# Optimization experiments

Measured on AMD Instinct MI355X. Metric: run time of the kernel, lower is better.

Reference implementation:

```python
import jax, jax.numpy as jnp
import numpy as np

N = 20000      # nodes
G = 400        # distinct TCR group ids
D_IN, H1, H2, D_OUT = 128, 256, 256, 128
LN_EPS = 1e-5


def _init_linear(key, fan_in, fan_out):
    s = 1.0 / np.sqrt(fan_in)
    return jax.random.uniform(key, (fan_in, fan_out), jnp.float32, -s, s)


def setup_inputs() -> dict:
    key = jax.random.key(0)
    ks = jax.random.split(key, 6)
    x = jax.random.normal(ks[0], (N, D_IN), jnp.float32)
    idx_TCR = jax.random.randint(ks[1], (N,), 0, G, dtype=jnp.int64)
    W1 = _init_linear(ks[2], D_IN, H1)
    W2 = _init_linear(ks[3], H1, H2)
    W3 = _init_linear(ks[4], H2, D_OUT)
    b1 = jnp.zeros((H1,), jnp.float32)
    b2 = jnp.zeros((H2,), jnp.float32)
    b3 = jnp.zeros((D_OUT,), jnp.float32)
    gamma = jnp.ones((D_OUT,), jnp.float32)
    beta = jnp.zeros((D_OUT,), jnp.float32)
    return {"x": x, "idx_TCR": idx_TCR, "W1": W1, "b1": b1,
            "W2": W2, "b2": b2, "W3": W3, "b3": b3,
            "gamma": gamma, "beta": beta}


def _build_edges(idx_TCR):
    # construct_graph: connect node pairs with equal idx, upper triangle only
    # (directed src<tgt edges, as in the torch code), then append self-loops
    # as PyG GCNConv.gcn_norm does.
    idx = np.asarray(idx_TCR).reshape(-1)
    n = idx.shape[0]
    eq = idx[:, None] == idx[None, :]
    src, tgt = np.nonzero(np.triu(eq, k=1))
    loop = np.arange(n)
    row = jnp.asarray(np.concatenate([src, loop]))  # message source
    col = jnp.asarray(np.concatenate([tgt, loop]))  # message target
    return row, col, n


def _gcn_norm(row, col, n, dtype):
    # degree from incoming edges (incl. self-loops), symmetric normalization
    deg = jax.ops.segment_sum(jnp.ones(row.shape[0], dtype), col, num_segments=n)
    dis = jnp.where(deg > 0, jax.lax.rsqrt(deg), jnp.zeros_like(deg))
    return dis[row] * dis[col]  # [E]


def _gcn_conv(x, W, b, row, col, norm, n):
    h = x @ W                                   # [N, out]
    msg = h[row] * norm[:, None]                # gather + scale, [E, out]
    out = jax.ops.segment_sum(msg, col, num_segments=n)  # scatter-add
    return out + b


def reference(x, idx_TCR, W1, b1, W2, b2, W3, b3, gamma, beta):
    row, col, n = _build_edges(idx_TCR)
    norm = _gcn_norm(row, col, n, x.dtype)
    h = jax.nn.relu(_gcn_conv(x, W1, b1, row, col, norm, n))
    h = jax.nn.relu(_gcn_conv(h, W2, b2, row, col, norm, n))
    h = jax.nn.relu(_gcn_conv(h, W3, b3, row, col, norm, n))
    # LayerNorm over last dim
    mu = h.mean(axis=-1, keepdims=True)
    var = ((h - mu) ** 2).mean(axis=-1, keepdims=True)
    return (h - mu) * jax.lax.rsqrt(var + LN_EPS) * gamma + beta
```

## Files before the change

### kernel.cpp

```cpp
#include <hip/hip_runtime.h>
#include <hip/hip_bf16.h>

#define NN 20000
#define NG 400
#define D_IN 128
#define H1 256
#define H2 256
#define D_OUT 128
#define MCAP 1024
#define WSLOT 256

#define STY 72
#define ST1 136
#define ST2 264
#define ST3 264
#define SF  132
#define REGB 36864

typedef __attribute__((ext_vector_type(8))) short short8;
typedef __attribute__((ext_vector_type(4))) short short4v;
typedef __attribute__((ext_vector_type(4))) float floatx4;

__device__ __forceinline__ short f2b(float f) {
    __hip_bfloat16 h = __float2bfloat16(f);
    return *(short*)&h;
}


__global__ __launch_bounds__(256) void wt_all_t(
    const float* __restrict__ W1, const float* __restrict__ W2,
    const float* __restrict__ W3, __hip_bfloat16* __restrict__ Wt1,
    __hip_bfloat16* __restrict__ Wt2, __hip_bfloat16* __restrict__ Wt3)
{
    __shared__ float tile[64][65];

    int bid = blockIdx.x;
    const float* W; __hip_bfloat16* Wt; int K, N, tk, tn;
    if (bid < 8)       { W = W1; Wt = Wt1; K = D_IN; N = H1;
                         tk = bid >> 2;        tn = bid & 3; }
    else if (bid < 24) { W = W2; Wt = Wt2; K = H1;   N = H2;
                         int b = bid - 8;  tk = b >> 2; tn = b & 3; }
    else               { W = W3; Wt = Wt3; K = H2;   N = D_OUT;
                         int b = bid - 24; tk = b >> 1; tn = b & 1; }

    int t = threadIdx.x;
    int c = t & 63;
    int r0 = t >> 6;
    int k0 = tk * 64, n0 = tn * 64;

#pragma unroll
    for (int it = 0; it < 16; ++it) {
        int r = r0 + it * 4;
        tile[r][c] = W[(size_t)(k0 + r) * N + n0 + c];
    }
    __syncthreads();

#pragma unroll
    for (int it = 0; it < 16; ++it) {
        int rn = r0 + it * 4;
        Wt[(size_t)(n0 + rn) * K + k0 + c] = __float2bfloat16(tile[c][rn]);
    }
}


__global__ __launch_bounds__(512) void fused_gcn(
    const float* __restrict__ x, const int* __restrict__ idx,
    const __hip_bfloat16* __restrict__ Wt1_,
    const __hip_bfloat16* __restrict__ Wt2_,
    const __hip_bfloat16* __restrict__ Wt3_,
    const float* __restrict__ b1, const float* __restrict__ b2,
    const float* __restrict__ b3,
    const float* __restrict__ gamma, const float* __restrict__ beta,
    float* __restrict__ out)
{
    __shared__ __align__(16) char RA[REGB];
    __shared__ __align__(16) char RB[REGB];
    __shared__ int mlist[MCAP];
    __shared__ int wcnt[8];

    int tid = threadIdx.x;
    int w = tid >> 6;
    int lane = tid & 63;
    int quad = lane >> 4;
    int l15 = lane & 15;
    int g = blockIdx.x;

    int* WS = (int*)RA;
    {
        int slice = w * 625;
        int wcount = 0;
        unsigned long long lowm = (1ull << lane) - 1ull;
#pragma unroll
        for (int b2i = 0; b2i < 2; ++b2i) {
            int4 v[5];
#pragma unroll
            for (int r = 0; r < 5; ++r) {
                int q = (b2i * 5 + r) * 64 + lane;
                v[r] = (q < 625) ? *(const int4*)&idx[(slice + q) * 4]
                                 : make_int4(-1, -1, -1, -1);
            }
#pragma unroll
            for (int r = 0; r < 5; ++r) {
                bool f0 = (v[r].x == g), f1 = (v[r].y == g);
                bool f2 = (v[r].z == g), f3 = (v[r].w == g);
                unsigned long long m0 = __ballot(f0), m1 = __ballot(f1);
                unsigned long long m2 = __ballot(f2), m3 = __ballot(f3);
                int p = wcount + __popcll(m0 & lowm) + __popcll(m1 & lowm)
                               + __popcll(m2 & lowm) + __popcll(m3 & lowm);
                int j0 = (slice + (b2i * 5 + r) * 64 + lane) * 4;
                int e0 = (int)f0, e1 = (int)f1, e2 = (int)f2;
                if (f0 && p < WSLOT)                WS[w * WSLOT + p] = j0;
                if (f1 && p + e0 < WSLOT)           WS[w * WSLOT + p + e0] = j0 + 1;
                if (f2 && p + e0 + e1 < WSLOT)      WS[w * WSLOT + p + e0 + e1] = j0 + 2;
                if (f3 && p + e0 + e1 + e2 < WSLOT) WS[w * WSLOT + p + e0 + e1 + e2] = j0 + 3;
                wcount += __popcll(m0) + __popcll(m1) + __popcll(m2) + __popcll(m3);
            }
        }
        if (lane == 0) wcnt[w] = min(wcount, WSLOT);
    }
    __syncthreads();
    int cnt = 0;
    {
        int myprefix = 0;
#pragma unroll
        for (int ww = 0; ww < 8; ++ww) {
            int c = wcnt[ww];
            if (ww < w) myprefix += c;
            cnt += c;
        }
        cnt = min(cnt, MCAP);
        int myc = wcnt[w];
        for (int k = lane; k < myc; k += 64) {
            int dstp = myprefix + k;
            if (dstp < MCAP) mlist[dstp] = WS[w * WSLOT + k];
        }
    }
    if (cnt <= 0) return;

    float2 gmv = *(const float2*)&gamma[lane * 2];
    float2 btv = *(const float2*)&beta[lane * 2];
    float4 bb1[2], bb2[2], bb3;
#pragma unroll
    for (int i = 0; i < 2; ++i) {
        bb1[i] = *(const float4*)&b1[(2 * w + i) * 16 + quad * 4];
        bb2[i] = *(const float4*)&b2[(2 * w + i) * 16 + quad * 4];
    }
    bb3 = *(const float4*)&b3[w * 16 + quad * 4];

    __syncthreads();

    auto ltfrag = [&](int nt, int k2) -> short8 {
        int thr = nt * 16 + l15 - k2 * 32 - quad * 8;
        short8 f;
#pragma unroll
        for (int e = 0; e < 8; ++e)
            f[e] = (e <= thr) ? (short)0x3F80 : (short)0;
        return f;
    };

    float c1[2][4], c2[2][4], c3[4];
#pragma unroll
    for (int r = 0; r < 4; ++r) {
        c1[0][r] = 0.f; c1[1][r] = 0.f;
        c2[0][r] = 0.f; c2[1][r] = 0.f;
        c3[r] = 0.f;
    }

    const short* wt1p = (const short*)Wt1_;
    const short* wt2p = (const short*)Wt2_;
    const short* wt3p = (const short*)Wt3_;

    for (int base = 0; base < cnt; base += 64) {
        asm("" : "+s"(wt1p), "+s"(wt2p), "+s"(wt3p));
        int mt = min(64, cnt - base);
        int par = (base >> 6) & 1;
        char* Rc = par ? RB : RA;
        char* Rd = par ? RA : RB;
        short* T1 = (short*)Rc;
        short* T2 = (short*)Rc;
        short* T3 = (short*)Rc;
        float* F  = (float*)Rc;
        short* Yt = (short*)Rd;

        float djn[4];
#pragma unroll
        for (int nt = 0; nt < 4; ++nt)
            djn[nt] = rsqrtf((float)(base + nt * 16 + l15 + 1));

        {
            int row = (lane >> 3) + 8 * w;
            int mr = base + row;
            int nid = mlist[mr < cnt ? mr : cnt - 1];
            float sdr = rsqrtf((float)(mr + 1));
            const float* xp = x + (size_t)nid * D_IN + (lane & 7) * 4;
#pragma unroll
            for (int t = 0; t < 4; ++t) {
                float4 v = *(const float4*)(xp + t * 32);
                short4v o;
                o[0] = f2b(v.x * sdr); o[1] = f2b(v.y * sdr);
                o[2] = f2b(v.z * sdr); o[3] = f2b(v.w * sdr);
                *(short4v*)&T1[row * ST1 + (lane & 7) * 4 + t * 32] = o;
            }
        }
        __syncthreads();

        {
            floatx4 acc[4][2];
#pragma unroll
            for (int i = 0; i < 4; ++i) { acc[i][0] = (floatx4)0.0f; acc[i][1] = (floatx4)0.0f; }
#pragma unroll
            for (int kk = 0; kk < 4; ++kk) {
                short8 a4[4], bw[2];
#pragma unroll
                for (int i = 0; i < 4; ++i)
                    a4[i] = *(const short8*)&T1[(i * 16 + l15) * ST1 + kk * 32 + quad * 8];
#pragma unroll
                for (int nt = 0; nt < 2; ++nt)
                    bw[nt] = *(const short8*)&wt1p[((size_t)((w * 2 + nt) * 16 + l15)) * D_IN + kk * 32 + quad * 8];
#pragma unroll
                for (int i = 0; i < 4; ++i)
#pragma unroll
                    for (int nt = 0; nt < 2; ++nt)
                        acc[i][nt] = __builtin_amdgcn_mfma_f32_16x16x32_bf16(
                            a4[i], bw[nt], acc[i][nt], 0, 0, 0);
            }
#pragma unroll
            for (int i = 0; i < 4; ++i)
#pragma unroll
                for (int nt = 0; nt < 2; ++nt) {
                    short4v o4;
#pragma unroll
                    for (int r = 0; r < 4; ++r) o4[r] = f2b(acc[i][nt][r]);
                    *(short4v*)&Yt[((w * 2 + nt) * 16 + l15) * STY + i * 16 + quad * 4] = o4;
                }
        }
        __syncthreads();

        {
            floatx4 acc[2][4];
#pragma unroll
            for (int i = 0; i < 2; ++i)
#pragma unroll
                for (int nt = 0; nt < 4; ++nt) acc[i][nt] = (floatx4)0.0f;
#pragma unroll
            for (int k2 = 0; k2 < 2; ++k2) {
                short8 af[2];
#pragma unroll
                for (int i = 0; i < 2; ++i)
                    af[i] = *(const short8*)&Yt[((2 * w + i) * 16 + l15) * STY + k2 * 32 + quad * 8];
#pragma unroll
                for (int nt = 0; nt < 4; ++nt) {
                    short8 lt = ltfrag(nt, k2);
#pragma unroll
                    for (int i = 0; i < 2; ++i)
                        acc[i][nt] = __builtin_amdgcn_mfma_f32_16x16x32_bf16(
                            af[i], lt, acc[i][nt], 0, 0, 0);
                }
            }
#pragma unroll
            for (int i = 0; i < 2; ++i) {
                float nc[4] = {0.f, 0.f, 0.f, 0.f};
#pragma unroll
                for (int nt = 0; nt < 4; ++nt) {
                    float tmp[4];
#pragma unroll
                    for (int r = 0; r < 4; ++r) tmp[r] = acc[i][nt][r] + c1[i][r];
                    if (nt == 3) {
#pragma unroll
                        for (int r = 0; r < 4; ++r) nc[r] = tmp[r];
                    }
                    short4v o4;
                    o4[0] = f2b(fmaxf(tmp[0] * djn[nt] + bb1[i].x, 0.0f) * djn[nt]);
                    o4[1] = f2b(fmaxf(tmp[1] * djn[nt] + bb1[i].y, 0.0f) * djn[nt]);
                    o4[2] = f2b(fmaxf(tmp[2] * djn[nt] + bb1[i].z, 0.0f) * djn[nt]);
                    o4[3] = f2b(fmaxf(tmp[3] * djn[nt] + bb1[i].w, 0.0f) * djn[nt]);
                    *(short4v*)&T2[(nt * 16 + l15) * ST2 + (2 * w + i) * 16 + quad * 4] = o4;
                }
#pragma unroll
                for (int r = 0; r < 4; ++r)
                    c1[i][r] = __shfl(nc[r], (lane & 48) + 15);
            }
        }
        __syncthreads();

        {
            floatx4 acc[4][2];
#pragma unroll
            for (int i = 0; i < 4; ++i) { acc[i][0] = (floatx4)0.0f; acc[i][1] = (floatx4)0.0f; }
#pragma unroll
            for (int kk = 0; kk < 8; ++kk) {
                short8 a4[4], bw[2];
#pragma unroll
                for (int i = 0; i < 4; ++i)
                    a4[i] = *(const short8*)&T2[(i * 16 + l15) * ST2 + kk * 32 + quad * 8];
#pragma unroll
                for (int nt = 0; nt < 2; ++nt)
                    bw[nt] = *(const short8*)&wt2p[((size_t)((w * 2 + nt) * 16 + l15)) * H1 + kk * 32 + quad * 8];
#pragma unroll
                for (int i = 0; i < 4; ++i)
#pragma unroll
                    for (int nt = 0; nt < 2; ++nt)
                        acc[i][nt] = __builtin_amdgcn_mfma_f32_16x16x32_bf16(
                            a4[i], bw[nt], acc[i][nt], 0, 0, 0);
            }
#pragma unroll
            for (int i = 0; i < 4; ++i)
#pragma unroll
                for (int nt = 0; nt < 2; ++nt) {
                    short4v o4;
#pragma unroll
                    for (int r = 0; r < 4; ++r) o4[r] = f2b(acc[i][nt][r]);
                    *(short4v*)&Yt[((w * 2 + nt) * 16 + l15) * STY + i * 16 + quad * 4] = o4;
                }
        }
        __syncthreads();

        {
            floatx4 acc[2][4];
#pragma unroll
            for (int i = 0; i < 2; ++i)
#pragma unroll
                for (int nt = 0; nt < 4; ++nt) acc[i][nt] = (floatx4)0.0f;
#pragma unroll
            for (int k2 = 0; k2 < 2; ++k2) {
                short8 af[2];
#pragma unroll
                for (int i = 0; i < 2; ++i)
                    af[i] = *(const short8*)&Yt[((2 * w + i) * 16 + l15) * STY + k2 * 32 + quad * 8];
#pragma unroll
                for (int nt = 0; nt < 4; ++nt) {
                    short8 lt = ltfrag(nt, k2);
#pragma unroll
                    for (int i = 0; i < 2; ++i)
                        acc[i][nt] = __builtin_amdgcn_mfma_f32_16x16x32_bf16(
                            af[i], lt, acc[i][nt], 0, 0, 0);
                }
            }
#pragma unroll
            for (int i = 0; i < 2; ++i) {
                float nc[4] = {0.f, 0.f, 0.f, 0.f};
#pragma unroll
                for (int nt = 0; nt < 4; ++nt) {
                    float tmp[4];
#pragma unroll
                    for (int r = 0; r < 4; ++r) tmp[r] = acc[i][nt][r] + c2[i][r];
                    if (nt == 3) {
#pragma unroll
                        for (int r = 0; r < 4; ++r) nc[r] = tmp[r];
                    }
                    short4v o4;
                    o4[0] = f2b(fmaxf(tmp[0] * djn[nt] + bb2[i].x, 0.0f) * djn[nt]);
                    o4[1] = f2b(fmaxf(tmp[1] * djn[nt] + bb2[i].y, 0.0f) * djn[nt]);
                    o4[2] = f2b(fmaxf(tmp[2] * djn[nt] + bb2[i].z, 0.0f) * djn[nt]);
                    o4[3] = f2b(fmaxf(tmp[3] * djn[nt] + bb2[i].w, 0.0f) * djn[nt]);
                    *(short4v*)&T3[(nt * 16 + l15) * ST3 + (2 * w + i) * 16 + quad * 4] = o4;
                }
#pragma unroll
                for (int r = 0; r < 4; ++r)
                    c2[i][r] = __shfl(nc[r], (lane & 48) + 15);
            }
        }
        __syncthreads();

        {
            floatx4 acc[4];
#pragma unroll
            for (int i = 0; i < 4; ++i) acc[i] = (floatx4)0.0f;
#pragma unroll
            for (int kk = 0; kk < 8; ++kk) {
                short8 bw = *(const short8*)&wt3p[((size_t)(w * 16 + l15)) * H2 + kk * 32 + quad * 8];
#pragma unroll
                for (int i = 0; i < 4; ++i) {
                    short8 a4 = *(const short8*)&T3[(i * 16 + l15) * ST3 + kk * 32 + quad * 8];
                    acc[i] = __builtin_amdgcn_mfma_f32_16x16x32_bf16(a4, bw, acc[i], 0, 0, 0);
                }
            }
#pragma unroll
            for (int i = 0; i < 4; ++i) {
                short4v o4;
#pragma unroll
                for (int r = 0; r < 4; ++r) o4[r] = f2b(acc[i][r]);
                *(short4v*)&Yt[(w * 16 + l15) * STY + i * 16 + quad * 4] = o4;
            }
        }
        __syncthreads();

        {
            floatx4 acc[4];
#pragma unroll
            for (int nt = 0; nt < 4; ++nt) acc[nt] = (floatx4)0.0f;
#pragma unroll
            for (int k2 = 0; k2 < 2; ++k2) {
                short8 af = *(const short8*)&Yt[(w * 16 + l15) * STY + k2 * 32 + quad * 8];
#pragma unroll
                for (int nt = 0; nt < 4; ++nt)
                    acc[nt] = __builtin_amdgcn_mfma_f32_16x16x32_bf16(
                        af, ltfrag(nt, k2), acc[nt], 0, 0, 0);
            }
            float nc[4] = {0.f, 0.f, 0.f, 0.f};
#pragma unroll
            for (int nt = 0; nt < 4; ++nt) {
                float tmp[4];
#pragma unroll
                for (int r = 0; r < 4; ++r) tmp[r] = acc[nt][r] + c3[r];
                if (nt == 3) {
#pragma unroll
                    for (int r = 0; r < 4; ++r) nc[r] = tmp[r];
                }
                float4 o;
                o.x = fmaxf(tmp[0] * djn[nt] + bb3.x, 0.0f);
                o.y = fmaxf(tmp[1] * djn[nt] + bb3.y, 0.0f);
                o.z = fmaxf(tmp[2] * djn[nt] + bb3.z, 0.0f);
                o.w = fmaxf(tmp[3] * djn[nt] + bb3.w, 0.0f);
                *(float4*)&F[(nt * 16 + l15) * SF + w * 16 + quad * 4] = o;
            }
#pragma unroll
            for (int r = 0; r < 4; ++r)
                c3[r] = __shfl(nc[r], (lane & 48) + 15);
        }
        __syncthreads();

        for (int r = w; r < mt; r += 8) {
            float2 v = *(const float2*)&F[r * SF + lane * 2];
            float s1 = v.x + v.y;
            float s2v = v.x * v.x + v.y * v.y;
#pragma unroll
            for (int off = 32; off > 0; off >>= 1) {
                s1 += __shfl_down(s1, off);
                s2v += __shfl_down(s2v, off);
            }
            s1 = __shfl(s1, 0);
            s2v = __shfl(s2v, 0);
            float mu = s1 * (1.0f / D_OUT);
            float var = s2v * (1.0f / D_OUT) - mu * mu;
            float rstd = rsqrtf(var + 1e-5f);
            float2 o;
            o.x = (v.x - mu) * rstd * gmv.x + btv.x;
            o.y = (v.y - mu) * rstd * gmv.y + btv.y;
            *(float2*)&out[(size_t)mlist[base + r] * D_OUT + lane * 2] = o;
        }
    }
}


extern "C" void kernel_launch(void* const* d_in, const int* in_sizes, int n_in,
                              void* d_out, int out_size, void* d_ws, size_t ws_size,
                              hipStream_t stream) {
    const float* x     = (const float*)d_in[0];
    const int*   idx   = (const int*)d_in[1];
    const float* W1    = (const float*)d_in[2];
    const float* b1    = (const float*)d_in[3];
    const float* W2    = (const float*)d_in[4];
    const float* b2    = (const float*)d_in[5];
    const float* W3    = (const float*)d_in[6];
    const float* b3    = (const float*)d_in[7];
    const float* gamma = (const float*)d_in[8];
    const float* beta  = (const float*)d_in[9];
    float* out = (float*)d_out;

    char* ws = (char*)d_ws;
    size_t off = 0;
    auto alloc = [&](size_t bytes) -> void* {
        void* p = (void*)(ws + off);
        off += (bytes + 255) & ~(size_t)255;
        return p;
    };
    __hip_bfloat16* Wt1 = (__hip_bfloat16*)alloc((size_t)D_IN * H1 * 2);
    __hip_bfloat16* Wt2 = (__hip_bfloat16*)alloc((size_t)H1 * H2 * 2);
    __hip_bfloat16* Wt3 = (__hip_bfloat16*)alloc((size_t)H2 * D_OUT * 2);

    wt_all_t<<<32, 256, 0, stream>>>(W1, W2, W3, Wt1, Wt2, Wt3);

    fused_gcn<<<NG, 512, 0, stream>>>(
        x, idx, Wt1, Wt2, Wt3, b1, b2, b3, gamma, beta, out);
}
```

Baseline: 127.4 us.

## Switch to persistent blocks with atomic work-stealing over TCR groups

Launches 256 persistent blocks instead of one block per group. After finishing a group, each block grabs the next group index from a global atomic counter that is zeroed by a memset before launch. This is meant to cut tail effects and per-block launch and setup costs across the 400 groups of uneven size. In exchange it adds a memset, one atomic per group and extra barriers, and every group still rescans the whole index array.

After: 127.9 us. No clear change (+0.4%).

```diff
diff --git a/kernel.cpp b/kernel.cpp
--- a/kernel.cpp
+++ b/kernel.cpp
@@ -9,6 +9,7 @@
 #define D_OUT 128
 #define MCAP 1024
 #define WSLOT 256
+#define GRID0 256
 
 #define STY 72
 #define ST1 136
@@ -54,7 +55,6 @@
         tile[r][c] = W[(size_t)(k0 + r) * N + n0 + c];
     }
     __syncthreads();
-
 #pragma unroll
     for (int it = 0; it < 16; ++it) {
         int rn = r0 + it * 4;
@@ -71,83 +71,27 @@
     const float* __restrict__ b1, const float* __restrict__ b2,
     const float* __restrict__ b3,
     const float* __restrict__ gamma, const float* __restrict__ beta,
-    float* __restrict__ out)
+    float* __restrict__ out, int* __restrict__ gctr)
 {
     __shared__ __align__(16) char RA[REGB];
     __shared__ __align__(16) char RB[REGB];
     __shared__ int mlist[MCAP];
     __shared__ int wcnt[8];
+    __shared__ int gsh;
 
     int tid = threadIdx.x;
     int w = tid >> 6;
     int lane = tid & 63;
     int quad = lane >> 4;
     int l15 = lane & 15;
-    int g = blockIdx.x;
-
-    int* WS = (int*)RA;
-    {
-        int slice = w * 625;
-        int wcount = 0;
-        unsigned long long lowm = (1ull << lane) - 1ull;
-#pragma unroll
-        for (int b2i = 0; b2i < 2; ++b2i) {
-            int4 v[5];
-#pragma unroll
-            for (int r = 0; r < 5; ++r) {
-                int q = (b2i * 5 + r) * 64 + lane;
-                v[r] = (q < 625) ? *(const int4*)&idx[(slice + q) * 4]
-                                 : make_int4(-1, -1, -1, -1);
-            }
-#pragma unroll
-            for (int r = 0; r < 5; ++r) {
-                bool f0 = (v[r].x == g), f1 = (v[r].y == g);
-                bool f2 = (v[r].z == g), f3 = (v[r].w == g);
-                unsigned long long m0 = __ballot(f0), m1 = __ballot(f1);
-                unsigned long long m2 = __ballot(f2), m3 = __ballot(f3);
-                int p = wcount + __popcll(m0 & lowm) + __popcll(m1 & lowm)
-                               + __popcll(m2 & lowm) + __popcll(m3 & lowm);
-                int j0 = (slice + (b2i * 5 + r) * 64 + lane) * 4;
-                int e0 = (int)f0, e1 = (int)f1, e2 = (int)f2;
-                if (f0 && p < WSLOT)                WS[w * WSLOT + p] = j0;
-                if (f1 && p + e0 < WSLOT)           WS[w * WSLOT + p + e0] = j0 + 1;
-                if (f2 && p + e0 + e1 < WSLOT)      WS[w * WSLOT + p + e0 + e1] = j0 + 2;
-                if (f3 && p + e0 + e1 + e2 < WSLOT) WS[w * WSLOT + p + e0 + e1 + e2] = j0 + 3;
-                wcount += __popcll(m0) + __popcll(m1) + __popcll(m2) + __popcll(m3);
-            }
-        }
-        if (lane == 0) wcnt[w] = min(wcount, WSLOT);
-    }
-    __syncthreads();
-    int cnt = 0;
-    {
-        int myprefix = 0;
-#pragma unroll
-        for (int ww = 0; ww < 8; ++ww) {
-            int c = wcnt[ww];
-            if (ww < w) myprefix += c;
-            cnt += c;
-        }
-        cnt = min(cnt, MCAP);
-        int myc = wcnt[w];
-        for (int k = lane; k < myc; k += 64) {
-            int dstp = myprefix + k;
-            if (dstp < MCAP) mlist[dstp] = WS[w * WSLOT + k];
-        }
-    }
-    if (cnt <= 0) return;
 
     float2 gmv = *(const float2*)&gamma[lane * 2];
     float2 btv = *(const float2*)&beta[lane * 2];
-    float4 bb1[2], bb2[2], bb3;
-#pragma unroll
-    for (int i = 0; i < 2; ++i) {
-        bb1[i] = *(const float4*)&b1[(2 * w + i) * 16 + quad * 4];
-        bb2[i] = *(const float4*)&b2[(2 * w + i) * 16 + quad * 4];
-    }
-    bb3 = *(const float4*)&b3[w * 16 + quad * 4];
-
-    __syncthreads();
+    float4 bb1a = *(const float4*)&b1[(2 * w + 0) * 16 + quad * 4];
+    float4 bb1b = *(const float4*)&b1[(2 * w + 1) * 16 + quad * 4];
+    float4 bb2a = *(const float4*)&b2[(2 * w + 0) * 16 + quad * 4];
+    float4 bb2b = *(const float4*)&b2[(2 * w + 1) * 16 + quad * 4];
+    float4 bb3  = *(const float4*)&b3[w * 16 + quad * 4];
 
     auto ltfrag = [&](int nt, int k2) -> short8 {
         int thr = nt * 16 + l15 - k2 * 32 - quad * 8;
@@ -158,287 +102,353 @@
         return f;
     };
 
-    float c1[2][4], c2[2][4], c3[4];
-#pragma unroll
-    for (int r = 0; r < 4; ++r) {
-        c1[0][r] = 0.f; c1[1][r] = 0.f;
-        c2[0][r] = 0.f; c2[1][r] = 0.f;
-        c3[r] = 0.f;
-    }
-
     const short* wt1p = (const short*)Wt1_;
     const short* wt2p = (const short*)Wt2_;
     const short* wt3p = (const short*)Wt3_;
 
-    for (int base = 0; base < cnt; base += 64) {
-        asm("" : "+s"(wt1p), "+s"(wt2p), "+s"(wt3p));
-        int mt = min(64, cnt - base);
-        int par = (base >> 6) & 1;
-        char* Rc = par ? RB : RA;
-        char* Rd = par ? RA : RB;
-        short* T1 = (short*)Rc;
-        short* T2 = (short*)Rc;
-        short* T3 = (short*)Rc;
-        float* F  = (float*)Rc;
-        short* Yt = (short*)Rd;
-
-        float djn[4];
-#pragma unroll
-        for (int nt = 0; nt < 4; ++nt)
-            djn[nt] = rsqrtf((float)(base + nt * 16 + l15 + 1));
-
+    int g = blockIdx.x;
+    while (g < NG) {
+        __syncthreads();
+
+        int* WS = (int*)RA;
         {
-            int row = (lane >> 3) + 8 * w;
-            int mr = base + row;
-            int nid = mlist[mr < cnt ? mr : cnt - 1];
-            float sdr = rsqrtf((float)(mr + 1));
-            const float* xp = x + (size_t)nid * D_IN + (lane & 7) * 4;
-#pragma unroll
-            for (int t = 0; t < 4; ++t) {
-                float4 v = *(const float4*)(xp + t * 32);
-                short4v o;
-                o[0] = f2b(v.x * sdr); o[1] = f2b(v.y * sdr);
-                o[2] = f2b(v.z * sdr); o[3] = f2b(v.w * sdr);
-                *(short4v*)&T1[row * ST1 + (lane & 7) * 4 + t * 32] = o;
+            int slice = w * 625;
+            int wcount = 0;
+            unsigned long long lowm = (1ull << lane) - 1ull;
+#pragma unroll
+            for (int b2i = 0; b2i < 2; ++b2i) {
+                int4 v[5];
+#pragma unroll
+                for (int r = 0; r < 5; ++r) {
+                    int q = (b2i * 5 + r) * 64 + lane;
+                    v[r] = (q < 625) ? *(const int4*)&idx[(slice + q) * 4]
+                                     : make_int4(-1, -1, -1, -1);
+                }
+#pragma unroll
+                for (int r = 0; r < 5; ++r) {
+                    bool f0 = (v[r].x == g), f1 = (v[r].y == g);
+                    bool f2 = (v[r].z == g), f3 = (v[r].w == g);
+                    unsigned long long m0 = __ballot(f0), m1 = __ballot(f1);
+                    unsigned long long m2 = __ballot(f2), m3 = __ballot(f3);
+                    int p = wcount + __popcll(m0 & lowm) + __popcll(m1 & lowm)
+                                   + __popcll(m2 & lowm) + __popcll(m3 & lowm);
+                    int j0 = (slice + (b2i * 5 + r) * 64 + lane) * 4;
+                    int e0 = (int)f0, e1 = (int)f1, e2 = (int)f2;
+                    if (f0 && p < WSLOT)                WS[w * WSLOT + p] = j0;
+                    if (f1 && p + e0 < WSLOT)           WS[w * WSLOT + p + e0] = j0 + 1;
+                    if (f2 && p + e0 + e1 < WSLOT)      WS[w * WSLOT + p + e0 + e1] = j0 + 2;
+                    if (f3 && p + e0 + e1 + e2 < WSLOT) WS[w * WSLOT + p + e0 + e1 + e2] = j0 + 3;
+                    wcount += __popcll(m0) + __popcll(m1) + __popcll(m2) + __popcll(m3);
+                }
+            }
+            if (lane == 0) wcnt[w] = min(wcount, WSLOT);
+        }
+        __syncthreads();
+        int cnt = 0;
+        {
+            int myprefix = 0;
+#pragma unroll
+            for (int ww = 0; ww < 8; ++ww) {
+                int c = wcnt[ww];
+                if (ww < w) myprefix += c;
+                cnt += c;
+            }
+            cnt = min(cnt, MCAP);
+            int myc = wcnt[w];
+            for (int k = lane; k < myc; k += 64) {
+                int dstp = myprefix + k;
+                if (dstp < MCAP) mlist[dstp] = WS[w * WSLOT + k];
             }
         }
-        __syncthreads();
-
-        {
-            floatx4 acc[4][2];
-#pragma unroll
-            for (int i = 0; i < 4; ++i) { acc[i][0] = (floatx4)0.0f; acc[i][1] = (floatx4)0.0f; }
-#pragma unroll
-            for (int kk = 0; kk < 4; ++kk) {
-                short8 a4[4], bw[2];
-#pragma unroll
-                for (int i = 0; i < 4; ++i)
-                    a4[i] = *(const short8*)&T1[(i * 16 + l15) * ST1 + kk * 32 + quad * 8];
-#pragma unroll
-                for (int nt = 0; nt < 2; ++nt)
-                    bw[nt] = *(const short8*)&wt1p[((size_t)((w * 2 + nt) * 16 + l15)) * D_IN + kk * 32 + quad * 8];
-#pragma unroll
-                for (int i = 0; i < 4; ++i)
-#pragma unroll
-                    for (int nt = 0; nt < 2; ++nt)
-                        acc[i][nt] = __builtin_amdgcn_mfma_f32_16x16x32_bf16(
-                            a4[i], bw[nt], acc[i][nt], 0, 0, 0);
+
+        if (cnt > 0) {
+            __syncthreads();
+
+            float c1[2][4], c2[2][4], c3[4];
+#pragma unroll
+            for (int r = 0; r < 4; ++r) {
+                c1[0][r] = 0.f; c1[1][r] = 0.f;
+                c2[0][r] = 0.f; c2[1][r] = 0.f;
+                c3[r] = 0.f;
             }
-#pragma unroll
-            for (int i = 0; i < 4; ++i)
-#pragma unroll
-                for (int nt = 0; nt < 2; ++nt) {
-                    short4v o4;
-#pragma unroll
-                    for (int r = 0; r < 4; ++r) o4[r] = f2b(acc[i][nt][r]);
-                    *(short4v*)&Yt[((w * 2 + nt) * 16 + l15) * STY + i * 16 + quad * 4] = o4;
-                }
-        }
-        __syncthreads();
-
-        {
-            floatx4 acc[2][4];
-#pragma unroll
-            for (int i = 0; i < 2; ++i)
-#pragma unroll
-                for (int nt = 0; nt < 4; ++nt) acc[i][nt] = (floatx4)0.0f;
-#pragma unroll
-            for (int k2 = 0; k2 < 2; ++k2) {
-                short8 af[2];
-#pragma unroll
-                for (int i = 0; i < 2; ++i)
-                    af[i] = *(const short8*)&Yt[((2 * w + i) * 16 + l15) * STY + k2 * 32 + quad * 8];
-#pragma unroll
-                for (int nt = 0; nt < 4; ++nt) {
-                    short8 lt = ltfrag(nt, k2);
+            float4 bb1[2] = {bb1a, bb1b};
+            float4 bb2[2] = {bb2a, bb2b};
+
+            for (int base = 0; base < cnt; base += 64) {
+                asm("" : "+s"(wt1p), "+s"(wt2p), "+s"(wt3p));
+                int mt = min(64, cnt - base);
+                int par = (base >> 6) & 1;
+                char* Rc = par ? RB : RA;
+                char* Rd = par ? RA : RB;
+                short* T1 = (short*)Rc;
+                short* T2 = (short*)Rc;
+                short* T3 = (short*)Rc;
+                float* F  = (float*)Rc;
+                short* Yt = (short*)Rd;
+
+                float djn[4];
+#pragma unroll
+                for (int nt = 0; nt < 4; ++nt)
+                    djn[nt] = rsqrtf((float)(base + nt * 16 + l15 + 1));
+
+                {
+                    int row = (lane >> 3) + 8 * w;
+                    int mr = base + row;
+                    int nid = mlist[mr < cnt ? mr : cnt - 1];
+                    float sdr = rsqrtf((float)(mr + 1));
+                    const float* xp = x + (size_t)nid * D_IN + (lane & 7) * 4;
+#pragma unroll
+                    for (int t = 0; t < 4; ++t) {
+                        float4 v = *(const float4*)(xp + t * 32);
+                        short4v o;
+                        o[0] = f2b(v.x * sdr); o[1] = f2b(v.y * sdr);
+                        o[2] = f2b(v.z * sdr); o[3] = f2b(v.w * sdr);
+                        *(short4v*)&T1[row * ST1 + (lane & 7) * 4 + t * 32] = o;
+                    }
+                }
+                __syncthreads();
+
+                {
+                    floatx4 acc[4][2];
+#pragma unroll
+                    for (int i = 0; i < 4; ++i) { acc[i][0] = (floatx4)0.0f; acc[i][1] = (floatx4)0.0f; }
+#pragma unroll
+                    for (int kk = 0; kk < 4; ++kk) {
+                        short8 a4[4], bw[2];
+#pragma unroll
+                        for (int i = 0; i < 4; ++i)
+                            a4[i] = *(const short8*)&T1[(i * 16 + l15) * ST1 + kk * 32 + quad * 8];
+#pragma unroll
+                        for (int nt = 0; nt < 2; ++nt)
+                            bw[nt] = *(const short8*)&wt1p[((size_t)((w * 2 + nt) * 16 + l15)) * D_IN + kk * 32 + quad * 8];
+#pragma unroll
+                        for (int i = 0; i < 4; ++i)
+#pragma unroll
+                            for (int nt = 0; nt < 2; ++nt)
+                                acc[i][nt] = __builtin_amdgcn_mfma_f32_16x16x32_bf16(
+                                    a4[i], bw[nt], acc[i][nt], 0, 0, 0);
+                    }
+#pragma unroll
+                    for (int i = 0; i < 4; ++i)
+#pragma unroll
+                        for (int nt = 0; nt < 2; ++nt) {
+                            short4v o4;
+#pragma unroll
+                            for (int r = 0; r < 4; ++r) o4[r] = f2b(acc[i][nt][r]);
+                            *(short4v*)&Yt[((w * 2 + nt) * 16 + l15) * STY + i * 16 + quad * 4] = o4;
+                        }
+                }
+                __syncthreads();
+
+                {
+                    floatx4 acc[2][4];
 #pragma unroll
                     for (int i = 0; i < 2; ++i)
-                        acc[i][nt] = __builtin_amdgcn_mfma_f32_16x16x32_bf16(
-                            af[i], lt, acc[i][nt], 0, 0, 0);
-                }
-            }
-#pragma unroll
-            for (int i = 0; i < 2; ++i) {
-                float nc[4] = {0.f, 0.f, 0.f, 0.f};
-#pragma unroll
-                for (int nt = 0; nt < 4; ++nt) {
-                    float tmp[4];
-#pragma unroll
-                    for (int r = 0; r < 4; ++r) tmp[r] = acc[i][nt][r] + c1[i][r];
-                    if (nt == 3) {
-#pragma unroll
-                        for (int r = 0; r < 4; ++r) nc[r] = tmp[r];
-                    }
-                    short4v o4;
-                    o4[0] = f2b(fmaxf(tmp[0] * djn[nt] + bb1[i].x, 0.0f) * djn[nt]);
-                    o4[1] = f2b(fmaxf(tmp[1] * djn[nt] + bb1[i].y, 0.0f) * djn[nt]);
-                    o4[2] = f2b(fmaxf(tmp[2] * djn[nt] + bb1[i].z, 0.0f) * djn[nt]);
-                    o4[3] = f2b(fmaxf(tmp[3] * djn[nt] + bb1[i].w, 0.0f) * djn[nt]);
-                    *(short4v*)&T2[(nt * 16 + l15) * ST2 + (2 * w + i) * 16 + quad * 4] = o4;
-                }
-#pragma unroll
-                for (int r = 0; r < 4; ++r)
-                    c1[i][r] = __shfl(nc[r], (lane & 48) + 15);
+#pragma unroll
+                        for (int nt = 0; nt < 4; ++nt) acc[i][nt] = (floatx4)0.0f;
+#pragma unroll
+                    for (int k2 = 0; k2 < 2; ++k2) {
+                        short8 af[2];
+#pragma unroll
+                        for (int i = 0; i < 2; ++i)
+                            af[i] = *(const short8*)&Yt[((2 * w + i) * 16 + l15) * STY + k2 * 32 + quad * 8];
+#pragma unroll
+                        for (int nt = 0; nt < 4; ++nt) {
+                            short8 lt = ltfrag(nt, k2);
+#pragma unroll
+                            for (int i = 0; i < 2; ++i)
+                                acc[i][nt] = __builtin_amdgcn_mfma_f32_16x16x32_bf16(
+                                    af[i], lt, acc[i][nt], 0, 0, 0);
+                        }
+                    }
+#pragma unroll
+                    for (int i = 0; i < 2; ++i) {
+                        float nc[4] = {0.f, 0.f, 0.f, 0.f};
+#pragma unroll
+                        for (int nt = 0; nt < 4; ++nt) {
+                            float tmp[4];
+#pragma unroll
+                            for (int r = 0; r < 4; ++r) tmp[r] = acc[i][nt][r] + c1[i][r];
+                            if (nt == 3) {
+#pragma unroll
+                                for (int r = 0; r < 4; ++r) nc[r] = tmp[r];
+                            }
+                            short4v o4;
+                            o4[0] = f2b(fmaxf(tmp[0] * djn[nt] + bb1[i].x, 0.0f) * djn[nt]);
+                            o4[1] = f2b(fmaxf(tmp[1] * djn[nt] + bb1[i].y, 0.0f) * djn[nt]);
+                            o4[2] = f2b(fmaxf(tmp[2] * djn[nt] + bb1[i].z, 0.0f) * djn[nt]);
+                            o4[3] = f2b(fmaxf(tmp[3] * djn[nt] + bb1[i].w, 0.0f) * djn[nt]);
+                            *(short4v*)&T2[(nt * 16 + l15) * ST2 + (2 * w + i) * 16 + quad * 4] = o4;
+                        }
+#pragma unroll
+                        for (int r = 0; r < 4; ++r)
+                            c1[i][r] = __shfl(nc[r], (lane & 48) + 15);
+                    }
+                }
+                __syncthreads();
+
+                {
+                    floatx4 acc[4][2];
+#pragma unroll
+                    for (int i = 0; i < 4; ++i) { acc[i][0] = (floatx4)0.0f; acc[i][1] = (floatx4)0.0f; }
+#pragma unroll
+                    for (int kk = 0; kk < 8; ++kk) {
+                        short8 a4[4], bw[2];
+#pragma unroll
+                        for (int i = 0; i < 4; ++i)
+                            a4[i] = *(const short8*)&T2[(i * 16 + l15) * ST2 + kk * 32 + quad * 8];
+#pragma unroll
+                        for (int nt = 0; nt < 2; ++nt)
+                            bw[nt] = *(const short8*)&wt2p[((size_t)((w * 2 + nt) * 16 + l15)) * H1 + kk * 32 + quad * 8];
+#pragma unroll
+                        for (int i = 0; i < 4; ++i)
+#pragma unroll
+                            for (int nt = 0; nt < 2; ++nt)
+                                acc[i][nt] = __builtin_amdgcn_mfma_f32_16x16x32_bf16(
+                                    a4[i], bw[nt], acc[i][nt], 0, 0, 0);
+                    }
+#pragma unroll
+                    for (int i = 0; i < 4; ++i)
+#pragma unroll
+                        for (int nt = 0; nt < 2; ++nt) {
+                            short4v o4;
+#pragma unroll
+                            for (int r = 0; r < 4; ++r) o4[r] = f2b(acc[i][nt][r]);
+                            *(short4v*)&Yt[((w * 2 + nt) * 16 + l15) * STY + i * 16 + quad * 4] = o4;
+                        }
+                }
+                __syncthreads();
+
+                {
+                    floatx4 acc[2][4];
+#pragma unroll
+                    for (int i = 0; i < 2; ++i)
+#pragma unroll
+                        for (int nt = 0; nt < 4; ++nt) acc[i][nt] = (floatx4)0.0f;
+#pragma unroll
+                    for (int k2 = 0; k2 < 2; ++k2) {
+                        short8 af[2];
+#pragma unroll
+                        for (int i = 0; i < 2; ++i)
+                            af[i] = *(const short8*)&Yt[((2 * w + i) * 16 + l15) * STY + k2 * 32 + quad * 8];
+#pragma unroll
+                        for (int nt = 0; nt < 4; ++nt) {
+                            short8 lt = ltfrag(nt, k2);
+#pragma unroll
+                            for (int i = 0; i < 2; ++i)
+                                acc[i][nt] = __builtin_amdgcn_mfma_f32_16x16x32_bf16(
+                                    af[i], lt, acc[i][nt], 0, 0, 0);
+                        }
+                    }
+#pragma unroll
+                    for (int i = 0; i < 2; ++i) {
+                        float nc[4] = {0.f, 0.f, 0.f, 0.f};
+#pragma unroll
+                        for (int nt = 0; nt < 4; ++nt) {
+                            float tmp[4];
+#pragma unroll
+                            for (int r = 0; r < 4; ++r) tmp[r] = acc[i][nt][r] + c2[i][r];
+                            if (nt == 3) {
+#pragma unroll
+                                for (int r = 0; r < 4; ++r) nc[r] = tmp[r];
+                            }
+                            short4v o4;
+                            o4[0] = f2b(fmaxf(tmp[0] * djn[nt] + bb2[i].x, 0.0f) * djn[nt]);
+                            o4[1] = f2b(fmaxf(tmp[1] * djn[nt] + bb2[i].y, 0.0f) * djn[nt]);
+                            o4[2] = f2b(fmaxf(tmp[2] * djn[nt] + bb2[i].z, 0.0f) * djn[nt]);
+                            o4[3] = f2b(fmaxf(tmp[3] * djn[nt] + bb2[i].w, 0.0f) * djn[nt]);
+                            *(short4v*)&T3[(nt * 16 + l15) * ST3 + (2 * w + i) * 16 + quad * 4] = o4;
+                        }
+#pragma unroll
+                        for (int r = 0; r < 4; ++r)
+                            c2[i][r] = __shfl(nc[r], (lane & 48) + 15);
+                    }
+                }
+                __syncthreads();
+
+                {
+                    floatx4 acc[4];
+#pragma unroll
+                    for (int i = 0; i < 4; ++i) acc[i] = (floatx4)0.0f;
+#pragma unroll
+                    for (int kk = 0; kk < 8; ++kk) {
+                        short8 bw = *(const short8*)&wt3p[((size_t)(w * 16 + l15)) * H2 + kk * 32 + quad * 8];
+#pragma unroll
+                        for (int i = 0; i < 4; ++i) {
+                            short8 a4 = *(const short8*)&T3[(i * 16 + l15) * ST3 + kk * 32 + quad * 8];
+                            acc[i] = __builtin_amdgcn_mfma_f32_16x16x32_bf16(a4, bw, acc[i], 0, 0, 0);
+                        }
+                    }
+#pragma unroll
+                    for (int i = 0; i < 4; ++i) {
+                        short4v o4;
+#pragma unroll
+                        for (int r = 0; r < 4; ++r) o4[r] = f2b(acc[i][r]);
+                        *(short4v*)&Yt[(w * 16 + l15) * STY + i * 16 + quad * 4] = o4;
+                    }
+                }
+                __syncthreads();
+
+                {
+                    floatx4 acc[4];
+#pragma unroll
+                    for (int nt = 0; nt < 4; ++nt) acc[nt] = (floatx4)0.0f;
+#pragma unroll
+                    for (int k2 = 0; k2 < 2; ++k2) {
+                        short8 af = *(const short8*)&Yt[(w * 16 + l15) * STY + k2 * 32 + quad * 8];
+#pragma unroll
+                        for (int nt = 0; nt < 4; ++nt)
+                            acc[nt] = __builtin_amdgcn_mfma_f32_16x16x32_bf16(
+                                af, ltfrag(nt, k2), acc[nt], 0, 0, 0);
+                    }
+                    float nc[4] = {0.f, 0.f, 0.f, 0.f};
+#pragma unroll
+                    for (int nt = 0; nt < 4; ++nt) {
+                        float tmp[4];
+#pragma unroll
+                        for (int r = 0; r < 4; ++r) tmp[r] = acc[nt][r] + c3[r];
+                        if (nt == 3) {
+#pragma unroll
+                            for (int r = 0; r < 4; ++r) nc[r] = tmp[r];
+                        }
+                        float4 o;
+                        o.x = fmaxf(tmp[0] * djn[nt] + bb3.x, 0.0f);
+                        o.y = fmaxf(tmp[1] * djn[nt] + bb3.y, 0.0f);
+                        o.z = fmaxf(tmp[2] * djn[nt] + bb3.z, 0.0f);
+                        o.w = fmaxf(tmp[3] * djn[nt] + bb3.w, 0.0f);
+                        *(float4*)&F[(nt * 16 + l15) * SF + w * 16 + quad * 4] = o;
+                    }
+#pragma unroll
+                    for (int r = 0; r < 4; ++r)
+                        c3[r] = __shfl(nc[r], (lane & 48) + 15);
+                }
+                __syncthreads();
+
+                for (int r = w; r < mt; r += 8) {
+                    float2 v = *(const float2*)&F[r * SF + lane * 2];
+                    float s1 = v.x + v.y;
+                    float s2v = v.x * v.x + v.y * v.y;
+#pragma unroll
+                    for (int off = 32; off > 0; off >>= 1) {
+                        s1 += __shfl_down(s1, off);
+                        s2v += __shfl_down(s2v, off);
+                    }
+                    s1 = __shfl(s1, 0);
+                    s2v = __shfl(s2v, 0);
+                    float mu = s1 * (1.0f / D_OUT);
+                    float var = s2v * (1.0f / D_OUT) - mu * mu;
+                    float rstd = rsqrtf(var + 1e-5f);
+                    float2 o;
+                    o.x = (v.x - mu) * rstd * gmv.x + btv.x;
+                    o.y = (v.y - mu) * rstd * gmv.y + btv.y;
+                    *(float2*)&out[(size_t)mlist[base + r] * D_OUT + lane * 2] = o;
+                }
             }
         }
+
+        if (tid == 0) gsh = GRID0 + atomicAdd(gctr, 1);
         __syncthreads();
-
-        {
-            floatx4 acc[4][2];
-#pragma unroll
-            for (int i = 0; i < 4; ++i) { acc[i][0] = (floatx4)0.0f; acc[i][1] = (floatx4)0.0f; }
-#pragma unroll
-            for (int kk = 0; kk < 8; ++kk) {
-                short8 a4[4], bw[2];
-#pragma unroll
-                for (int i = 0; i < 4; ++i)
-                    a4[i] = *(const short8*)&T2[(i * 16 + l15) * ST2 + kk * 32 + quad * 8];
-#pragma unroll
-                for (int nt = 0; nt < 2; ++nt)
-                    bw[nt] = *(const short8*)&wt2p[((size_t)((w * 2 + nt) * 16 + l15)) * H1 + kk * 32 + quad * 8];
-#pragma unroll
-                for (int i = 0; i < 4; ++i)
-#pragma unroll
-                    for (int nt = 0; nt < 2; ++nt)
-                        acc[i][nt] = __builtin_amdgcn_mfma_f32_16x16x32_bf16(
-                            a4[i], bw[nt], acc[i][nt], 0, 0, 0);
-            }
-#pragma unroll
-            for (int i = 0; i < 4; ++i)
-#pragma unroll
-                for (int nt = 0; nt < 2; ++nt) {
-                    short4v o4;
-#pragma unroll
-                    for (int r = 0; r < 4; ++r) o4[r] = f2b(acc[i][nt][r]);
-                    *(short4v*)&Yt[((w * 2 + nt) * 16 + l15) * STY + i * 16 + quad * 4] = o4;
-                }
-        }
-        __syncthreads();
-
-        {
-            floatx4 acc[2][4];
-#pragma unroll
-            for (int i = 0; i < 2; ++i)
-#pragma unroll
-                for (int nt = 0; nt < 4; ++nt) acc[i][nt] = (floatx4)0.0f;
-#pragma unroll
-            for (int k2 = 0; k2 < 2; ++k2) {
-                short8 af[2];
-#pragma unroll
-                for (int i = 0; i < 2; ++i)
-                    af[i] = *(const short8*)&Yt[((2 * w + i) * 16 + l15) * STY + k2 * 32 + quad * 8];
-#pragma unroll
-                for (int nt = 0; nt < 4; ++nt) {
-                    short8 lt = ltfrag(nt, k2);
-#pragma unroll
-                    for (int i = 0; i < 2; ++i)
-                        acc[i][nt] = __builtin_amdgcn_mfma_f32_16x16x32_bf16(
-                            af[i], lt, acc[i][nt], 0, 0, 0);
-                }
-            }
-#pragma unroll
-            for (int i = 0; i < 2; ++i) {
-                float nc[4] = {0.f, 0.f, 0.f, 0.f};
-#pragma unroll
-                for (int nt = 0; nt < 4; ++nt) {
-                    float tmp[4];
-#pragma unroll
-                    for (int r = 0; r < 4; ++r) tmp[r] = acc[i][nt][r] + c2[i][r];
-                    if (nt == 3) {
-#pragma unroll
-                        for (int r = 0; r < 4; ++r) nc[r] = tmp[r];
-                    }
-                    short4v o4;
-                    o4[0] = f2b(fmaxf(tmp[0] * djn[nt] + bb2[i].x, 0.0f) * djn[nt]);
-                    o4[1] = f2b(fmaxf(tmp[1] * djn[nt] + bb2[i].y, 0.0f) * djn[nt]);
-                    o4[2] = f2b(fmaxf(tmp[2] * djn[nt] + bb2[i].z, 0.0f) * djn[nt]);
-                    o4[3] = f2b(fmaxf(tmp[3] * djn[nt] + bb2[i].w, 0.0f) * djn[nt]);
-                    *(short4v*)&T3[(nt * 16 + l15) * ST3 + (2 * w + i) * 16 + quad * 4] = o4;
-                }
-#pragma unroll
-                for (int r = 0; r < 4; ++r)
-                    c2[i][r] = __shfl(nc[r], (lane & 48) + 15);
-            }
-        }
-        __syncthreads();
-
-        {
-            floatx4 acc[4];
-#pragma unroll
-            for (int i = 0; i < 4; ++i) acc[i] = (floatx4)0.0f;
-#pragma unroll
-            for (int kk = 0; kk < 8; ++kk) {
-                short8 bw = *(const short8*)&wt3p[((size_t)(w * 16 + l15)) * H2 + kk * 32 + quad * 8];
-#pragma unroll
-                for (int i = 0; i < 4; ++i) {
-                    short8 a4 = *(const short8*)&T3[(i * 16 + l15) * ST3 + kk * 32 + quad * 8];
-                    acc[i] = __builtin_amdgcn_mfma_f32_16x16x32_bf16(a4, bw, acc[i], 0, 0, 0);
-                }
-            }
-#pragma unroll
-            for (int i = 0; i < 4; ++i) {
-                short4v o4;
-#pragma unroll
-                for (int r = 0; r < 4; ++r) o4[r] = f2b(acc[i][r]);
-                *(short4v*)&Yt[(w * 16 + l15) * STY + i * 16 + quad * 4] = o4;
-            }
-        }
-        __syncthreads();
-
-        {
-            floatx4 acc[4];
-#pragma unroll
-            for (int nt = 0; nt < 4; ++nt) acc[nt] = (floatx4)0.0f;
-#pragma unroll
-            for (int k2 = 0; k2 < 2; ++k2) {
-                short8 af = *(const short8*)&Yt[(w * 16 + l15) * STY + k2 * 32 + quad * 8];
-#pragma unroll
-                for (int nt = 0; nt < 4; ++nt)
-                    acc[nt] = __builtin_amdgcn_mfma_f32_16x16x32_bf16(
-                        af, ltfrag(nt, k2), acc[nt], 0, 0, 0);
-            }
-            float nc[4] = {0.f, 0.f, 0.f, 0.f};
-#pragma unroll
-            for (int nt = 0; nt < 4; ++nt) {
-                float tmp[4];
-#pragma unroll
-                for (int r = 0; r < 4; ++r) tmp[r] = acc[nt][r] + c3[r];
-                if (nt == 3) {
-#pragma unroll
-                    for (int r = 0; r < 4; ++r) nc[r] = tmp[r];
-                }
-                float4 o;
-                o.x = fmaxf(tmp[0] * djn[nt] + bb3.x, 0.0f);
-                o.y = fmaxf(tmp[1] * djn[nt] + bb3.y, 0.0f);
-                o.z = fmaxf(tmp[2] * djn[nt] + bb3.z, 0.0f);
-                o.w = fmaxf(tmp[3] * djn[nt] + bb3.w, 0.0f);
-                *(float4*)&F[(nt * 16 + l15) * SF + w * 16 + quad * 4] = o;
-            }
-#pragma unroll
-            for (int r = 0; r < 4; ++r)
-                c3[r] = __shfl(nc[r], (lane & 48) + 15);
-        }
-        __syncthreads();
-
-        for (int r = w; r < mt; r += 8) {
-            float2 v = *(const float2*)&F[r * SF + lane * 2];
-            float s1 = v.x + v.y;
-            float s2v = v.x * v.x + v.y * v.y;
-#pragma unroll
-            for (int off = 32; off > 0; off >>= 1) {
-                s1 += __shfl_down(s1, off);
-                s2v += __shfl_down(s2v, off);
-            }
-            s1 = __shfl(s1, 0);
-            s2v = __shfl(s2v, 0);
-            float mu = s1 * (1.0f / D_OUT);
-            float var = s2v * (1.0f / D_OUT) - mu * mu;
-            float rstd = rsqrtf(var + 1e-5f);
-            float2 o;
-            o.x = (v.x - mu) * rstd * gmv.x + btv.x;
-            o.y = (v.y - mu) * rstd * gmv.y + btv.y;
-            *(float2*)&out[(size_t)mlist[base + r] * D_OUT + lane * 2] = o;
-        }
+        g = gsh;
     }
 }
 
@@ -468,9 +478,11 @@
     __hip_bfloat16* Wt1 = (__hip_bfloat16*)alloc((size_t)D_IN * H1 * 2);
     __hip_bfloat16* Wt2 = (__hip_bfloat16*)alloc((size_t)H1 * H2 * 2);
     __hip_bfloat16* Wt3 = (__hip_bfloat16*)alloc((size_t)H2 * D_OUT * 2);
+    int* gctr = (int*)alloc(256);
 
     wt_all_t<<<32, 256, 0, stream>>>(W1, W2, W3, Wt1, Wt2, Wt3);
-
-    fused_gcn<<<NG, 512, 0, stream>>>(
-        x, idx, Wt1, Wt2, Wt3, b1, b2, b3, gamma, beta, out);
+    hipMemsetAsync(gctr, 0, sizeof(int), stream);
+
+    fused_gcn<<<GRID0, 512, 0, stream>>>(
+        x, idx, Wt1, Wt2, Wt3, b1, b2, b3, gamma, beta, out, gctr);
 }
```
